# Kernel optimization log

Measured on AMD Instinct MI355X. Metric: run time of the kernel, lower is better.

Reference implementation:

```python
import jax, jax.numpy as jnp
import numpy as np

B, S, H, L = 4096, 64, 768, 5
TEMP = 0.07
BN_EPS = 1e-5


def setup_inputs() -> dict:
    key = jax.random.key(0)
    ks = jax.random.split(key, 8)
    seq = jax.random.normal(ks[0], (B, S, H), dtype=jnp.float32)
    labels = jax.random.randint(ks[1], (B,), 0, L)
    s = 1.0 / np.sqrt(H)
    return {
        'sequence_output': seq,
        'cls_gamma': jnp.ones((H,), jnp.float32),
        'cls_beta': jnp.zeros((H,), jnp.float32),
        'cls_W': jax.random.normal(ks[2], (H, H), jnp.float32) * s,
        'cls_b': jax.random.normal(ks[3], (H,), jnp.float32) * 0.01,
        'label_gamma': jnp.ones((H,), jnp.float32),
        'label_beta': jnp.zeros((H,), jnp.float32),
        'label_W': jax.random.normal(ks[4], (H, H), jnp.float32) * s,
        'label_b': jax.random.normal(ks[5], (H,), jnp.float32) * 0.01,
        'labels': labels,
    }


def _batchnorm(x, gamma, beta):
    # training-mode BatchNorm1d: biased batch stats
    m = x.mean(0)
    v = jnp.mean((x - m) ** 2, axis=0)
    return (x - m) * jax.lax.rsqrt(v + BN_EPS) * gamma + beta


def _l2norm(x):
    return x / jnp.sqrt(jnp.sum(x * x, axis=-1, keepdims=True)).clip(1e-12)


def reference(sequence_output, cls_gamma, cls_beta, cls_W, cls_b,
              label_gamma, label_beta, label_W, label_b, labels):
    z = sequence_output[:, 0, :]  # [B,H]; dropout is identity in eval
    # label token spans: 'No relation' -> positions 1:3 (mean), rest single tokens 3..6
    theta = jnp.stack([
        sequence_output[:, 1:3, :].mean(axis=1),
        sequence_output[:, 3, :],
        sequence_output[:, 4, :],
        sequence_output[:, 5, :],
        sequence_output[:, 6, :],
    ], axis=1)  # [B,L,H]
    z_cl, theta_cl = z, theta

    zp = _batchnorm(z, cls_gamma, cls_beta) @ cls_W.T + cls_b  # [B,H]
    tp = _batchnorm(theta.reshape(-1, H), label_gamma, label_beta) @ label_W.T + label_b
    tp = tp.reshape(-1, L, H)  # [B,L,H]
    logits = jnp.einsum('blh,bh->bl', tp, zp)  # [B,L]

    # ---- dual supervised contrastive loss (vectorized over the python loops) ----
    z_norm = _l2norm(z_cl)        # [B,H]
    theta_norm = _l2norm(theta_cl)  # [B,L,H]
    same = labels[:, None] == labels[None, :]          # [B,B]
    eye = jnp.eye(labels.shape[0], dtype=bool)
    pos_mask = (same & ~eye).astype(jnp.float32)       # positives (same label, j != i)
    neg_mask = (~same).astype(jnp.float32)             # negatives (different label)
    has_pos = (same & ~eye).any(axis=1)

    # l_z: anchor z_i vs theta_j[labels_i] (pos) and all theta_j[:] for diff-label j (neg)
    expS = jnp.exp(jnp.einsum('ih,jlh->ijl', z_norm, theta_norm) / TEMP)  # [B,B,L]
    expS_at_lab = jnp.take_along_axis(
        expS, jnp.broadcast_to(labels[:, None, None], expS.shape[:2] + (1,)), axis=2
    )[..., 0]  # expS[i,j,labels[i]] -> [B,B]
    pos_z = jnp.sum(expS_at_lab * pos_mask, axis=1)
    neg_z = jnp.sum(expS.sum(axis=-1) * neg_mask, axis=1)
    l_z = jnp.where(has_pos, -jnp.log(pos_z / (pos_z + neg_z + 1e-8)), 0.0).sum()

    # l_theta: anchor theta_i[labels_i] vs z_j
    anchor_theta = jnp.take_along_axis(theta_norm, labels[:, None, None], axis=1)[:, 0, :]  # [B,H]
    expT = jnp.exp(anchor_theta @ z_norm.T / TEMP)  # [B,B]
    pos_t = jnp.sum(expT * pos_mask, axis=1)
    neg_t = jnp.sum(expT * neg_mask, axis=1)
    l_t = jnp.where(has_pos, -jnp.log(pos_t / (pos_t + neg_t + 1e-8)), 0.0).sum()

    dual_loss = (l_z + l_t) / labels.shape[0]
    return logits, dual_loss
```

## Files before the change

kernel.cpp:

```cpp
#include <hip/hip_runtime.h>
#include <hip/hip_bf16.h>
#include <cstdint>
#include <cstddef>

#define B_N 4096
#define S_N 64
#define H_N 768
#define L_N 5
#define TEMP_INV (1.0f / 0.07f)
#define BN_EPS 1e-5f

typedef __attribute__((ext_vector_type(8))) short short8;
typedef __attribute__((ext_vector_type(4))) float f32x4;

__device__ __forceinline__ void async_copy16(void* lds, const void* g) {
  __builtin_amdgcn_global_load_lds(
      (const __attribute__((address_space(1))) unsigned int*)g,
      (__attribute__((address_space(3))) unsigned int*)lds, 16, 0, 0);
}

__device__ __forceinline__ unsigned short bf16b(float x) {
  __hip_bfloat16 h = __float2bfloat16(x);
  return *reinterpret_cast<unsigned short*>(&h);
}
__device__ __forceinline__ void store_bf16x4(void* p, float4 v) {
  ushort4 o = make_ushort4(bf16b(v.x), bf16b(v.y), bf16b(v.z), bf16b(v.w));
  *reinterpret_cast<ushort4*>(p) = o;
}

__device__ inline float block_reduce_sum256(float v, float* sbuf) {
#pragma unroll
  for (int off = 32; off > 0; off >>= 1) v += __shfl_down(v, off, 64);
  int lane = threadIdx.x & 63;
  int wid = threadIdx.x >> 6;
  __syncthreads();
  if (lane == 0) sbuf[wid] = v;
  __syncthreads();
  float r = 0.f;
  if (threadIdx.x == 0) r = sbuf[0] + sbuf[1] + sbuf[2] + sbuf[3];
  return r;
}

__global__ __launch_bounds__(256) void extract_kernel(
    const float* __restrict__ seq, __hip_bfloat16* __restrict__ zb,
    __hip_bfloat16* __restrict__ tb, float* __restrict__ zn_inv,
    float* __restrict__ thn_inv, float* __restrict__ sum_z,
    float* __restrict__ ssq_z, float* __restrict__ sum_t,
    float* __restrict__ ssq_t) {
  __shared__ float pr[8][6][3];
  int t = threadIdx.x;
  int wv = t >> 6, ln = t & 63;
  bool act = t < 192;
  int c4 = t * 4;
  int b0 = blockIdx.x * 8;
  float zs[4] = {}, zq[4] = {}, ts4[4] = {}, tq4[4] = {};
  for (int r = 0; r < 8; ++r) {
    int b = b0 + r;
    const float* base = seq + (size_t)b * (S_N * H_N);
    float pv[6] = {0.f, 0.f, 0.f, 0.f, 0.f, 0.f};
    if (act) {
      float4 z4 = *(const float4*)(base + c4);
      store_bf16x4(zb + (size_t)b * H_N + c4, z4);
      pv[0] = z4.x * z4.x + z4.y * z4.y + z4.z * z4.z + z4.w * z4.w;
      zs[0] += z4.x; zs[1] += z4.y; zs[2] += z4.z; zs[3] += z4.w;
      zq[0] += z4.x * z4.x; zq[1] += z4.y * z4.y;
      zq[2] += z4.z * z4.z; zq[3] += z4.w * z4.w;
#pragma unroll
      for (int l = 0; l < L_N; ++l) {
        float4 v4;
        if (l == 0) {
          float4 a4 = *(const float4*)(base + H_N + c4);
          float4 b4 = *(const float4*)(base + 2 * H_N + c4);
          v4 = make_float4(0.5f * (a4.x + b4.x), 0.5f * (a4.y + b4.y),
                           0.5f * (a4.z + b4.z), 0.5f * (a4.w + b4.w));
        } else {
          v4 = *(const float4*)(base + (size_t)(l + 2) * H_N + c4);
        }
        store_bf16x4(tb + ((size_t)b * L_N + l) * H_N + c4, v4);
        pv[1 + l] = v4.x * v4.x + v4.y * v4.y + v4.z * v4.z + v4.w * v4.w;
        ts4[0] += v4.x; ts4[1] += v4.y; ts4[2] += v4.z; ts4[3] += v4.w;
        tq4[0] += v4.x * v4.x; tq4[1] += v4.y * v4.y;
        tq4[2] += v4.z * v4.z; tq4[3] += v4.w * v4.w;
      }
    }
#pragma unroll
    for (int v = 0; v < 6; ++v) {
      float x = pv[v];
#pragma unroll
      for (int off = 32; off > 0; off >>= 1) x += __shfl_down(x, off, 64);
      if (ln == 0 && wv < 3) pr[r][v][wv] = x;
    }
  }
  __syncthreads();
  if (t < 48) {
    int r = t / 6, v = t - r * 6;
    float s = pr[r][v][0] + pr[r][v][1] + pr[r][v][2];
    float inv = 1.f / fmaxf(sqrtf(s), 1e-12f);
    int b = b0 + r;
    if (v == 0) zn_inv[b] = inv;
    else thn_inv[b * L_N + (v - 1)] = inv;
  }
  if (act) {
#pragma unroll
    for (int j = 0; j < 4; ++j) {
      atomicAdd(&sum_z[c4 + j], zs[j]);
      atomicAdd(&ssq_z[c4 + j], zq[j]);
      atomicAdd(&sum_t[c4 + j], ts4[j]);
      atomicAdd(&ssq_t[c4 + j], tq4[j]);
    }
  }
}

__global__ void count_kernel(const int* __restrict__ labels, int* __restrict__ cnt) {
  int i = blockIdx.x * 256 + threadIdx.x;
  if (i < B_N) atomicAdd(&cnt[labels[i]], 1);
}

__global__ void finalize_kernel(
    const float* __restrict__ sum_z, const float* __restrict__ ssq_z,
    const float* __restrict__ sum_t, const float* __restrict__ ssq_t,
    const float* __restrict__ g_z, const float* __restrict__ b_z,
    const float* __restrict__ g_t, const float* __restrict__ b_t,
    float* __restrict__ sz_s, float* __restrict__ sz_t,
    float* __restrict__ st_s, float* __restrict__ st_t) {
  int h = blockIdx.x * 256 + threadIdx.x;
  if (h >= H_N) return;
  {
    float m = sum_z[h] * (1.f / B_N);
    float v = ssq_z[h] * (1.f / B_N) - m * m;
    float s = g_z[h] * rsqrtf(v + BN_EPS);
    sz_s[h] = s;
    sz_t[h] = b_z[h] - m * s;
  }
  {
    float m = sum_t[h] * (1.f / (B_N * L_N));
    float v = ssq_t[h] * (1.f / (B_N * L_N)) - m * m;
    float s = g_t[h] * rsqrtf(v + BN_EPS);
    st_s[h] = s;
    st_t[h] = b_t[h] - m * s;
  }
}

__global__ __launch_bounds__(256) void prep_cls_kernel(
    const float* __restrict__ W, const float* __restrict__ szs,
    const float* __restrict__ szt, const float* __restrict__ bias,
    __hip_bfloat16* __restrict__ Wb, float* __restrict__ cprime) {
  __shared__ float sbuf[4];
  int n = blockIdx.x;
  int t = threadIdx.x;
  float dot = 0.f;
  if (t < 192) {
    int c4 = t * 4;
    const float* row = W + (size_t)n * H_N;
    float4 w4 = *(const float4*)(row + c4);
    float4 s4 = *(const float4*)(szs + c4);
    float4 t4 = *(const float4*)(szt + c4);
    store_bf16x4(Wb + (size_t)n * H_N + c4,
                 make_float4(w4.x * s4.x, w4.y * s4.y, w4.z * s4.z, w4.w * s4.w));
    dot = w4.x * t4.x + w4.y * t4.y + w4.z * t4.z + w4.w * t4.w;
  }
  float s = block_reduce_sum256(dot, sbuf);
  if (t == 0) cprime[n] = s + bias[n];
}

__global__ __launch_bounds__(256) void transpose_wl_kernel(
    const float* __restrict__ Wl, __hip_bfloat16* __restrict__ WlT) {
  __shared__ float tile[32][33];
  int t = threadIdx.x;
  int tx = t & 31, ty0 = t >> 5;
  int n0 = blockIdx.x * 32, k0 = blockIdx.y * 32;
#pragma unroll
  for (int p = 0; p < 4; ++p)
    tile[ty0 + p * 8][tx] = Wl[(size_t)(n0 + ty0 + p * 8) * H_N + k0 + tx];
  __syncthreads();
#pragma unroll
  for (int p = 0; p < 4; ++p) {
    unsigned short us = bf16b(tile[tx][ty0 + p * 8]);
    *((unsigned short*)WlT + (size_t)(k0 + ty0 + p * 8) * H_N + n0 + tx) = us;
  }
}

template <bool WRITE_BF16, bool HAS_BIAS>
__global__ __launch_bounds__(256) void gemm128_kernel(
    const __hip_bfloat16* __restrict__ A, const __hip_bfloat16* __restrict__ Bm,
    const float* __restrict__ bias, float* __restrict__ outF,
    __hip_bfloat16* __restrict__ outB) {
  __shared__ __align__(16) __hip_bfloat16 Asm[128 * 32];
  __shared__ __align__(16) __hip_bfloat16 Bsm[128 * 32];
  int tid = threadIdx.x, lane = tid & 63, wid = tid >> 6;
  int wr = wid >> 1, wc = wid & 1;
  int i0 = blockIdx.x * 128, n0 = blockIdx.y * 128;
  int llo = lane & 15, lhi = lane >> 4;
  f32x4 acc[4][4] = {};
  for (int k0 = 0; k0 < H_N; k0 += 32) {
#pragma unroll
    for (int r = 0; r < 2; ++r) {
      int s = r * 256 + wid * 64 + lane;
      int row = s >> 2, kc = (s & 3) * 8;
      size_t go = (size_t)row * H_N + k0 + kc;
      async_copy16((char*)Asm + (size_t)(r * 256 + wid * 64) * 16,
                   A + (size_t)i0 * H_N + go);
      async_copy16((char*)Bsm + (size_t)(r * 256 + wid * 64) * 16,
                   Bm + (size_t)n0 * H_N + go);
    }
    __syncthreads();
    short8 a[4], b[4];
#pragma unroll
    for (int m = 0; m < 4; ++m)
      a[m] = *(const short8*)((const char*)Asm +
                              ((wr * 64 + m * 16 + llo) * 32 + lhi * 8) * 2);
#pragma unroll
    for (int n = 0; n < 4; ++n)
      b[n] = *(const short8*)((const char*)Bsm +
                              ((wc * 64 + n * 16 + llo) * 32 + lhi * 8) * 2);
#pragma unroll
    for (int m = 0; m < 4; ++m)
#pragma unroll
      for (int n = 0; n < 4; ++n)
        acc[m][n] =
            __builtin_amdgcn_mfma_f32_16x16x32_bf16(a[m], b[n], acc[m][n], 0, 0, 0);
    __syncthreads();
  }
#pragma unroll
  for (int n = 0; n < 4; ++n) {
    int col = n0 + wc * 64 + n * 16 + llo;
    float bv = HAS_BIAS ? bias[col] : 0.f;
#pragma unroll
    for (int m = 0; m < 4; ++m) {
#pragma unroll
      for (int r = 0; r < 4; ++r) {
        int row = i0 + wr * 64 + m * 16 + lhi * 4 + r;
        float val = acc[m][n][r] + bv;
        outF[(size_t)row * H_N + col] = val;
        if (WRITE_BF16)
          outB[(size_t)row * H_N + col] = __float2bfloat16(val);
      }
    }
  }
}

__global__ __launch_bounds__(256) void logits_kernel(
    const float* __restrict__ seq, const float* __restrict__ u,
    const float* __restrict__ zp, const float* __restrict__ st_s,
    const float* __restrict__ st_t, const float* __restrict__ label_b,
    float* __restrict__ out) {
  __shared__ float sbuf[4];
  int b = blockIdx.x;
  int t = threadIdx.x;
  bool act = t < 192;
  int c4 = t * 4;
  float4 w4 = make_float4(0.f, 0.f, 0.f, 0.f);
  float apart = 0.f;
  if (act) {
    float4 u4 = *(const float4*)(u + (size_t)b * H_N + c4);
    float4 zp4 = *(const float4*)(zp + (size_t)b * H_N + c4);
    float4 ss4 = *(const float4*)(st_s + c4);
    float4 tt4 = *(const float4*)(st_t + c4);
    float4 lb4 = *(const float4*)(label_b + c4);
    w4 = make_float4(u4.x * ss4.x, u4.y * ss4.y, u4.z * ss4.z, u4.w * ss4.w);
    apart = u4.x * tt4.x + u4.y * tt4.y + u4.z * tt4.z + u4.w * tt4.w +
            zp4.x * lb4.x + zp4.y * lb4.y + zp4.z * lb4.z + zp4.w * lb4.w;
  }
  float alpha = block_reduce_sum256(apart, sbuf);
  const float* base = seq + (size_t)b * (S_N * H_N);
#pragma unroll
  for (int l = 0; l < L_N; ++l) {
    float part = 0.f;
    if (act) {
      float4 v4;
      if (l == 0) {
        float4 a4 = *(const float4*)(base + H_N + c4);
        float4 b4 = *(const float4*)(base + 2 * H_N + c4);
        v4 = make_float4(0.5f * (a4.x + b4.x), 0.5f * (a4.y + b4.y),
                         0.5f * (a4.z + b4.z), 0.5f * (a4.w + b4.w));
      } else {
        v4 = *(const float4*)(base + (size_t)(l + 2) * H_N + c4);
      }
      part = v4.x * w4.x + v4.y * w4.y + v4.z * w4.z + v4.w * w4.w;
    }
    float s = block_reduce_sum256(part, sbuf);
    if (t == 0) out[b * L_N + l] = s + alpha;
  }
}

#define NT_K 24
__global__ __launch_bounds__(256, 3) void sgemm_fused_kernel(
    const __hip_bfloat16* __restrict__ zb, const __hip_bfloat16* __restrict__ tb,
    const float* __restrict__ zn_inv, const float* __restrict__ thn_inv,
    const int* __restrict__ labels, float* __restrict__ pos_z,
    float* __restrict__ neg_z, float* __restrict__ pos_t,
    float* __restrict__ neg_t) {
  __shared__ __align__(128) char ldsbuf[2][16384];

  const int tid = threadIdx.x;
  const int lane = tid & 63, wid = tid >> 6;
  const int llo = lane & 15, lhi = lane >> 4;
  const int wr = wid >> 1, wc = wid & 1;
  const int xcd = blockIdx.x & 7;
  const int s0 = blockIdx.x >> 3;
  const int i0 = (xcd * 4 + (s0 & 3)) * 128;
  const int n0 = (s0 >> 2) * 128;

  f32x4 acc[4][4] = {};

  auto stage = [&](int c, int kt) {
#pragma unroll
    for (int h = 0; h < 2; ++h) {
      int s = h * 256 + tid;
      int R = s >> 3, sp = s & 7;
      int l = sp ^ (R & 7);
      int grow = 2 * R + (l >> 2);
      int gk = kt * 32 + (l & 3) * 8;
      int wub = (h * 256 + wid * 64) * 16;
      async_copy16(&ldsbuf[c][0] + wub, zb + (size_t)(i0 + grow) * H_N + gk);
      async_copy16(&ldsbuf[c][8192] + wub, tb + (size_t)(n0 + grow) * H_N + gk);
    }
  };

  auto fragOff = [&](int r) {
    int R = r >> 1;
    int slot = (r & 1) * 4 + lhi;
    return R * 128 + ((slot ^ (R & 7)) * 16);
  };

  stage(0, 0);
  asm volatile("s_waitcnt vmcnt(0)" ::: "memory");
  __builtin_amdgcn_s_barrier();

  for (int t = 0; t < NT_K; ++t) {
    if (t + 1 < NT_K) stage((t + 1) & 1, t + 1);
    const char* A = &ldsbuf[t & 1][0];
    const char* B = &ldsbuf[t & 1][8192];
    short8 a[4], b[4];
#pragma unroll
    for (int m = 0; m < 4; ++m) a[m] = *(const short8*)(A + fragOff(wr * 64 + m * 16 + llo));
#pragma unroll
    for (int n = 0; n < 4; ++n) b[n] = *(const short8*)(B + fragOff(wc * 64 + n * 16 + llo));
    asm volatile("s_waitcnt lgkmcnt(0)" ::: "memory");
    __builtin_amdgcn_sched_barrier(0);
    __builtin_amdgcn_s_setprio(1);
#pragma unroll
    for (int m = 0; m < 4; ++m)
#pragma unroll
      for (int n = 0; n < 4; ++n)
        acc[m][n] =
            __builtin_amdgcn_mfma_f32_16x16x32_bf16(a[m], b[n], acc[m][n], 0, 0, 0);
    __builtin_amdgcn_s_setprio(0);
    asm volatile("s_waitcnt vmcnt(0)" ::: "memory");
    __builtin_amdgcn_s_barrier();
  }
  __syncthreads();

  float* rpos = (float*)&ldsbuf[0][0];
  float* rneg = rpos + 128;
  float* cpos = rneg + 128;
  float* cneg = cpos + 128;
  float* rnorm = cneg + 128;
  float* cnorm = rnorm + 128;
  int* rowlab = (int*)(cnorm + 128);
  int* colj = rowlab + 128;
  int* coll = colj + 128;
  int* collab = coll + 128;

  if (tid < 128) {
    rowlab[tid] = labels[i0 + tid];
    rnorm[tid] = zn_inv[i0 + tid] * TEMP_INV;
    int c = n0 + tid;
    int j = c / 5;
    colj[tid] = j;
    coll[tid] = c - j * 5;
    collab[tid] = labels[j];
    cnorm[tid] = thn_inv[c];
    rpos[tid] = 0.f; rneg[tid] = 0.f; cpos[tid] = 0.f; cneg[tid] = 0.f;
  }
  __syncthreads();

  int cl[4], jg[4], lv[4], lj[4];
  float cs[4];
#pragma unroll
  for (int ni = 0; ni < 4; ++ni) {
    cl[ni] = wc * 64 + ni * 16 + llo;
    jg[ni] = colj[cl[ni]];
    lv[ni] = coll[cl[ni]];
    lj[ni] = collab[cl[ni]];
    cs[ni] = cnorm[cl[ni]];
  }
  float cpAcc[4] = {}, cnAcc[4] = {};
#pragma unroll
  for (int mi = 0; mi < 4; ++mi) {
#pragma unroll
    for (int r = 0; r < 4; ++r) {
      int rl = wr * 64 + mi * 16 + lhi * 4 + r;
      int ig = i0 + rl;
      int li = rowlab[rl];
      float rscale = rnorm[rl];
      float rp = 0.f, rn = 0.f;
#pragma unroll
      for (int ni = 0; ni < 4; ++ni) {
        float e = __expf(acc[mi][ni][r] * rscale * cs[ni]);
        bool same = (li == lj[ni]);
        bool diag = (ig == jg[ni]);
        if (same) {
          if (!diag && lv[ni] == li) { rp += e; cpAcc[ni] += e; }
        } else {
          rn += e;
          if (lv[ni] == lj[ni]) cnAcc[ni] += e;
        }
      }
      if (rp != 0.f) atomicAdd(&rpos[rl], rp);
      if (rn != 0.f) atomicAdd(&rneg[rl], rn);
    }
  }
#pragma unroll
  for (int ni = 0; ni < 4; ++ni) {
    if (cpAcc[ni] != 0.f) atomicAdd(&cpos[cl[ni]], cpAcc[ni]);
    if (cnAcc[ni] != 0.f) atomicAdd(&cneg[cl[ni]], cnAcc[ni]);
  }
  __syncthreads();
  if (tid < 128) {
    float v;
    v = rpos[tid]; if (v != 0.f) atomicAdd(&pos_z[i0 + tid], v);
    v = rneg[tid]; if (v != 0.f) atomicAdd(&neg_z[i0 + tid], v);
    int j = colj[tid];
    v = cpos[tid]; if (v != 0.f) atomicAdd(&pos_t[j], v);
    v = cneg[tid]; if (v != 0.f) atomicAdd(&neg_t[j], v);
  }
}

__global__ __launch_bounds__(256) void loss_kernel(
    const float* __restrict__ pos_z, const float* __restrict__ neg_z,
    const float* __restrict__ pos_t, const float* __restrict__ neg_t,
    const int* __restrict__ labels, const int* __restrict__ cnt,
    float* __restrict__ out_loss) {
  __shared__ float sbuf[4];
  int i = blockIdx.x * 256 + threadIdx.x;
  float term = 0.f;
  int li = labels[i];
  if (cnt[li] > 1) {
    float pz = pos_z[i], nz = neg_z[i];
    float pt = pos_t[i], nt = neg_t[i];
    term = -logf(pz / (pz + nz + 1e-8f)) - logf(pt / (pt + nt + 1e-8f));
  }
  float s = block_reduce_sum256(term, sbuf);
  if (threadIdx.x == 0) atomicAdd(out_loss, s * (1.0f / B_N));
}

extern "C" void kernel_launch(void* const* d_in, const int* in_sizes, int n_in,
                              void* d_out, int out_size, void* d_ws, size_t ws_size,
                              hipStream_t stream) {
  const float* seq = (const float*)d_in[0];
  const float* cls_gamma = (const float*)d_in[1];
  const float* cls_beta = (const float*)d_in[2];
  const float* cls_W = (const float*)d_in[3];
  const float* cls_b = (const float*)d_in[4];
  const float* label_gamma = (const float*)d_in[5];
  const float* label_beta = (const float*)d_in[6];
  const float* label_W = (const float*)d_in[7];
  const float* label_b = (const float*)d_in[8];
  const int* labels = (const int*)d_in[9];
  float* out = (float*)d_out;
  float* ws = (float*)d_ws;

  constexpr size_t OFF_SUMZ = 0;
  constexpr size_t OFF_SSQZ = 768;
  constexpr size_t OFF_SUMT = 1536;
  constexpr size_t OFF_SSQT = 2304;
  constexpr size_t OFF_POSZ = 3072;
  constexpr size_t OFF_NEGZ = 7168;
  constexpr size_t OFF_POST = 11264;
  constexpr size_t OFF_NEGT = 15360;
  constexpr size_t OFF_CNT = 19456;
  constexpr size_t ZERO_FLOATS = 19464;
  constexpr size_t OFF_SZS = 19464;
  constexpr size_t OFF_SZT = 20232;
  constexpr size_t OFF_STS = 21000;
  constexpr size_t OFF_STT = 21768;
  constexpr size_t OFF_ZNI = 22536;
  constexpr size_t OFF_TNI = 26632;
  constexpr size_t OFF_CPRIME = 47112;
  constexpr size_t OFF_ZP = 47880;
  constexpr size_t OFF_U = OFF_ZP + (size_t)B_N * H_N;
  constexpr size_t F32_END = OFF_U + (size_t)B_N * H_N;
  constexpr size_t BYTE_ZB = F32_END * sizeof(float);
  constexpr size_t BYTE_TB = BYTE_ZB + (size_t)B_N * H_N * 2;
  constexpr size_t BYTE_ZPB = BYTE_TB + (size_t)B_N * L_N * H_N * 2;
  constexpr size_t BYTE_WCB = BYTE_ZPB + (size_t)B_N * H_N * 2;
  constexpr size_t BYTE_WLT = BYTE_WCB + (size_t)H_N * H_N * 2;
  constexpr size_t TOTAL_BYTES = BYTE_WLT + (size_t)H_N * H_N * 2;
  if (ws_size < TOTAL_BYTES) return;

  __hip_bfloat16* zb = (__hip_bfloat16*)((char*)d_ws + BYTE_ZB);
  __hip_bfloat16* tb = (__hip_bfloat16*)((char*)d_ws + BYTE_TB);
  __hip_bfloat16* zpb = (__hip_bfloat16*)((char*)d_ws + BYTE_ZPB);
  __hip_bfloat16* wcb = (__hip_bfloat16*)((char*)d_ws + BYTE_WCB);
  __hip_bfloat16* wlt = (__hip_bfloat16*)((char*)d_ws + BYTE_WLT);

  hipMemsetAsync(d_ws, 0, ZERO_FLOATS * sizeof(float), stream);
  hipMemsetAsync((char*)d_out + (size_t)B_N * L_N * sizeof(float), 0, sizeof(float),
                 stream);

  extract_kernel<<<512, 256, 0, stream>>>(seq, zb, tb, ws + OFF_ZNI, ws + OFF_TNI,
                                          ws + OFF_SUMZ, ws + OFF_SSQZ,
                                          ws + OFF_SUMT, ws + OFF_SSQT);
  count_kernel<<<16, 256, 0, stream>>>(labels, (int*)(ws + OFF_CNT));
  finalize_kernel<<<3, 256, 0, stream>>>(
      ws + OFF_SUMZ, ws + OFF_SSQZ, ws + OFF_SUMT, ws + OFF_SSQT, cls_gamma,
      cls_beta, label_gamma, label_beta, ws + OFF_SZS, ws + OFF_SZT, ws + OFF_STS,
      ws + OFF_STT);
  prep_cls_kernel<<<H_N, 256, 0, stream>>>(cls_W, ws + OFF_SZS, ws + OFF_SZT, cls_b,
                                           wcb, ws + OFF_CPRIME);
  transpose_wl_kernel<<<dim3(24, 24), 256, 0, stream>>>(label_W, wlt);
  gemm128_kernel<true, true><<<dim3(32, 6), 256, 0, stream>>>(
      zb, wcb, ws + OFF_CPRIME, ws + OFF_ZP, zpb);
  gemm128_kernel<false, false><<<dim3(32, 6), 256, 0, stream>>>(
      zpb, wlt, nullptr, ws + OFF_U, nullptr);
  logits_kernel<<<B_N, 256, 0, stream>>>(seq, ws + OFF_U, ws + OFF_ZP, ws + OFF_STS,
                                         ws + OFF_STT, label_b, out);
  sgemm_fused_kernel<<<5120, 256, 0, stream>>>(
      zb, tb, ws + OFF_ZNI, ws + OFF_TNI, labels, ws + OFF_POSZ, ws + OFF_NEGZ,
      ws + OFF_POST, ws + OFF_NEGT);
  loss_kernel<<<16, 256, 0, stream>>>(ws + OFF_POSZ, ws + OFF_NEGZ, ws + OFF_POST,
                                      ws + OFF_NEGT, labels,
                                      (const int*)(ws + OFF_CNT),
                                      out + (size_t)B_N * L_N);
}
```

Baseline: 461.1 us.

## Shrink sgemm column tile, fuse label count into extract, read bf16 theta in logits

```diff
diff --git a/kernel.cpp b/kernel.cpp
--- a/kernel.cpp
+++ b/kernel.cpp
@@ -27,6 +27,10 @@
   ushort4 o = make_ushort4(bf16b(v.x), bf16b(v.y), bf16b(v.z), bf16b(v.w));
   *reinterpret_cast<ushort4*>(p) = o;
 }
+__device__ __forceinline__ float bf2f(unsigned short u) {
+  unsigned int x = ((unsigned int)u) << 16;
+  return *reinterpret_cast<float*>(&x);
+}
 
 __device__ inline float block_reduce_sum256(float v, float* sbuf) {
 #pragma unroll
@@ -46,13 +50,15 @@
     __hip_bfloat16* __restrict__ tb, float* __restrict__ zn_inv,
     float* __restrict__ thn_inv, float* __restrict__ sum_z,
     float* __restrict__ ssq_z, float* __restrict__ sum_t,
-    float* __restrict__ ssq_t) {
+    float* __restrict__ ssq_t, const int* __restrict__ labels,
+    int* __restrict__ cnt) {
   __shared__ float pr[8][6][3];
   int t = threadIdx.x;
   int wv = t >> 6, ln = t & 63;
   bool act = t < 192;
   int c4 = t * 4;
   int b0 = blockIdx.x * 8;
+  if (t < 8) atomicAdd(&cnt[labels[b0 + t]], 1);
   float zs[4] = {}, zq[4] = {}, ts4[4] = {}, tq4[4] = {};
   for (int r = 0; r < 8; ++r) {
     int b = b0 + r;
@@ -109,11 +115,6 @@
       atomicAdd(&ssq_t[c4 + j], tq4[j]);
     }
   }
-}
-
-__global__ void count_kernel(const int* __restrict__ labels, int* __restrict__ cnt) {
-  int i = blockIdx.x * 256 + threadIdx.x;
-  if (i < B_N) atomicAdd(&cnt[labels[i]], 1);
 }
 
 __global__ void finalize_kernel(
@@ -240,7 +241,7 @@
 }
 
 __global__ __launch_bounds__(256) void logits_kernel(
-    const float* __restrict__ seq, const float* __restrict__ u,
+    const __hip_bfloat16* __restrict__ tb, const float* __restrict__ u,
     const float* __restrict__ zp, const float* __restrict__ st_s,
     const float* __restrict__ st_t, const float* __restrict__ label_b,
     float* __restrict__ out) {
@@ -262,21 +263,14 @@
             zp4.x * lb4.x + zp4.y * lb4.y + zp4.z * lb4.z + zp4.w * lb4.w;
   }
   float alpha = block_reduce_sum256(apart, sbuf);
-  const float* base = seq + (size_t)b * (S_N * H_N);
 #pragma unroll
   for (int l = 0; l < L_N; ++l) {
     float part = 0.f;
     if (act) {
-      float4 v4;
-      if (l == 0) {
-        float4 a4 = *(const float4*)(base + H_N + c4);
-        float4 b4 = *(const float4*)(base + 2 * H_N + c4);
-        v4 = make_float4(0.5f * (a4.x + b4.x), 0.5f * (a4.y + b4.y),
-                         0.5f * (a4.z + b4.z), 0.5f * (a4.w + b4.w));
-      } else {
-        v4 = *(const float4*)(base + (size_t)(l + 2) * H_N + c4);
-      }
-      part = v4.x * w4.x + v4.y * w4.y + v4.z * w4.z + v4.w * w4.w;
+      ushort4 tv = *(const ushort4*)((const unsigned short*)tb +
+                                     ((size_t)b * L_N + l) * H_N + c4);
+      part = bf2f(tv.x) * w4.x + bf2f(tv.y) * w4.y + bf2f(tv.z) * w4.z +
+             bf2f(tv.w) * w4.w;
     }
     float s = block_reduce_sum256(part, sbuf);
     if (t == 0) out[b * L_N + l] = s + alpha;
@@ -284,13 +278,13 @@
 }
 
 #define NT_K 24
-__global__ __launch_bounds__(256, 3) void sgemm_fused_kernel(
+__global__ __launch_bounds__(256, 4) void sgemm_fused_kernel(
     const __hip_bfloat16* __restrict__ zb, const __hip_bfloat16* __restrict__ tb,
     const float* __restrict__ zn_inv, const float* __restrict__ thn_inv,
     const int* __restrict__ labels, float* __restrict__ pos_z,
     float* __restrict__ neg_z, float* __restrict__ pos_t,
     float* __restrict__ neg_t) {
-  __shared__ __align__(128) char ldsbuf[2][16384];
+  __shared__ __align__(128) char ldsbuf[2][12288];
 
   const int tid = threadIdx.x;
   const int lane = tid & 63, wid = tid >> 6;
@@ -299,9 +293,9 @@
   const int xcd = blockIdx.x & 7;
   const int s0 = blockIdx.x >> 3;
   const int i0 = (xcd * 4 + (s0 & 3)) * 128;
-  const int n0 = (s0 >> 2) * 128;
-
-  f32x4 acc[4][4] = {};
+  const int n0 = (s0 >> 2) * 64;
+
+  f32x4 acc[4][2] = {};
 
   auto stage = [&](int c, int kt) {
 #pragma unroll
@@ -313,6 +307,14 @@
       int gk = kt * 32 + (l & 3) * 8;
       int wub = (h * 256 + wid * 64) * 16;
       async_copy16(&ldsbuf[c][0] + wub, zb + (size_t)(i0 + grow) * H_N + gk);
+    }
+    {
+      int s = tid;
+      int R = s >> 3, sp = s & 7;
+      int l = sp ^ (R & 7);
+      int grow = 2 * R + (l >> 2);
+      int gk = kt * 32 + (l & 3) * 8;
+      int wub = (wid * 64) * 16;
       async_copy16(&ldsbuf[c][8192] + wub, tb + (size_t)(n0 + grow) * H_N + gk);
     }
   };
@@ -331,18 +333,20 @@
     if (t + 1 < NT_K) stage((t + 1) & 1, t + 1);
     const char* A = &ldsbuf[t & 1][0];
     const char* B = &ldsbuf[t & 1][8192];
-    short8 a[4], b[4];
-#pragma unroll
-    for (int m = 0; m < 4; ++m) a[m] = *(const short8*)(A + fragOff(wr * 64 + m * 16 + llo));
-#pragma unroll
-    for (int n = 0; n < 4; ++n) b[n] = *(const short8*)(B + fragOff(wc * 64 + n * 16 + llo));
+    short8 a[4], b[2];
+#pragma unroll
+    for (int m = 0; m < 4; ++m)
+      a[m] = *(const short8*)(A + fragOff(wr * 64 + m * 16 + llo));
+#pragma unroll
+    for (int n = 0; n < 2; ++n)
+      b[n] = *(const short8*)(B + fragOff(wc * 32 + n * 16 + llo));
     asm volatile("s_waitcnt lgkmcnt(0)" ::: "memory");
     __builtin_amdgcn_sched_barrier(0);
     __builtin_amdgcn_s_setprio(1);
 #pragma unroll
     for (int m = 0; m < 4; ++m)
 #pragma unroll
-      for (int n = 0; n < 4; ++n)
+      for (int n = 0; n < 2; ++n)
         acc[m][n] =
             __builtin_amdgcn_mfma_f32_16x16x32_bf16(a[m], b[n], acc[m][n], 0, 0, 0);
     __builtin_amdgcn_s_setprio(0);
@@ -353,39 +357,42 @@
 
   float* rpos = (float*)&ldsbuf[0][0];
   float* rneg = rpos + 128;
-  float* cpos = rneg + 128;
-  float* cneg = cpos + 128;
-  float* rnorm = cneg + 128;
-  float* cnorm = rnorm + 128;
-  int* rowlab = (int*)(cnorm + 128);
+  float* rnorm = rneg + 128;
+  float* cpos = rnorm + 128;
+  float* cneg = cpos + 64;
+  float* cnorm = cneg + 64;
+  int* rowlab = (int*)(cnorm + 64);
   int* colj = rowlab + 128;
-  int* coll = colj + 128;
-  int* collab = coll + 128;
+  int* coll = colj + 64;
+  int* collab = coll + 64;
 
   if (tid < 128) {
     rowlab[tid] = labels[i0 + tid];
     rnorm[tid] = zn_inv[i0 + tid] * TEMP_INV;
+    rpos[tid] = 0.f; rneg[tid] = 0.f;
+  }
+  if (tid < 64) {
     int c = n0 + tid;
     int j = c / 5;
     colj[tid] = j;
     coll[tid] = c - j * 5;
     collab[tid] = labels[j];
     cnorm[tid] = thn_inv[c];
-    rpos[tid] = 0.f; rneg[tid] = 0.f; cpos[tid] = 0.f; cneg[tid] = 0.f;
-  }
-  __syncthreads();
-
-  int cl[4], jg[4], lv[4], lj[4];
-  float cs[4];
-#pragma unroll
-  for (int ni = 0; ni < 4; ++ni) {
-    cl[ni] = wc * 64 + ni * 16 + llo;
+    cpos[tid] = 0.f; cneg[tid] = 0.f;
+  }
+  __syncthreads();
+
+  int cl[2], jg[2], lv[2], lj[2];
+  float cs[2];
+#pragma unroll
+  for (int ni = 0; ni < 2; ++ni) {
+    cl[ni] = wc * 32 + ni * 16 + llo;
     jg[ni] = colj[cl[ni]];
     lv[ni] = coll[cl[ni]];
     lj[ni] = collab[cl[ni]];
     cs[ni] = cnorm[cl[ni]];
   }
-  float cpAcc[4] = {}, cnAcc[4] = {};
+  float cpAcc[2] = {}, cnAcc[2] = {};
 #pragma unroll
   for (int mi = 0; mi < 4; ++mi) {
 #pragma unroll
@@ -396,7 +403,7 @@
       float rscale = rnorm[rl];
       float rp = 0.f, rn = 0.f;
 #pragma unroll
-      for (int ni = 0; ni < 4; ++ni) {
+      for (int ni = 0; ni < 2; ++ni) {
         float e = __expf(acc[mi][ni][r] * rscale * cs[ni]);
         bool same = (li == lj[ni]);
         bool diag = (ig == jg[ni]);
@@ -412,7 +419,7 @@
     }
   }
 #pragma unroll
-  for (int ni = 0; ni < 4; ++ni) {
+  for (int ni = 0; ni < 2; ++ni) {
     if (cpAcc[ni] != 0.f) atomicAdd(&cpos[cl[ni]], cpAcc[ni]);
     if (cnAcc[ni] != 0.f) atomicAdd(&cneg[cl[ni]], cnAcc[ni]);
   }
@@ -421,7 +428,10 @@
     float v;
     v = rpos[tid]; if (v != 0.f) atomicAdd(&pos_z[i0 + tid], v);
     v = rneg[tid]; if (v != 0.f) atomicAdd(&neg_z[i0 + tid], v);
+  }
+  if (tid < 64) {
     int j = colj[tid];
+    float v;
     v = cpos[tid]; if (v != 0.f) atomicAdd(&pos_t[j], v);
     v = cneg[tid]; if (v != 0.f) atomicAdd(&neg_t[j], v);
   }
@@ -501,8 +511,8 @@
 
   extract_kernel<<<512, 256, 0, stream>>>(seq, zb, tb, ws + OFF_ZNI, ws + OFF_TNI,
                                           ws + OFF_SUMZ, ws + OFF_SSQZ,
-                                          ws + OFF_SUMT, ws + OFF_SSQT);
-  count_kernel<<<16, 256, 0, stream>>>(labels, (int*)(ws + OFF_CNT));
+                                          ws + OFF_SUMT, ws + OFF_SSQT, labels,
+                                          (int*)(ws + OFF_CNT));
   finalize_kernel<<<3, 256, 0, stream>>>(
       ws + OFF_SUMZ, ws + OFF_SSQZ, ws + OFF_SUMT, ws + OFF_SSQT, cls_gamma,
       cls_beta, label_gamma, label_beta, ws + OFF_SZS, ws + OFF_SZT, ws + OFF_STS,
@@ -514,9 +524,9 @@
       zb, wcb, ws + OFF_CPRIME, ws + OFF_ZP, zpb);
   gemm128_kernel<false, false><<<dim3(32, 6), 256, 0, stream>>>(
       zpb, wlt, nullptr, ws + OFF_U, nullptr);
-  logits_kernel<<<B_N, 256, 0, stream>>>(seq, ws + OFF_U, ws + OFF_ZP, ws + OFF_STS,
+  logits_kernel<<<B_N, 256, 0, stream>>>(tb, ws + OFF_U, ws + OFF_ZP, ws + OFF_STS,
                                          ws + OFF_STT, label_b, out);
-  sgemm_fused_kernel<<<5120, 256, 0, stream>>>(
+  sgemm_fused_kernel<<<10240, 256, 0, stream>>>(
       zb, tb, ws + OFF_ZNI, ws + OFF_TNI, labels, ws + OFF_POSZ, ws + OFF_NEGZ,
       ws + OFF_POST, ws + OFF_NEGT);
   loss_kernel<<<16, 256, 0, stream>>>(ws + OFF_POSZ, ws + OFF_NEGZ, ws + OFF_POST,
```

New measurement: 601.6 us. 30.5% more time.

## Trim idle threads, fuse label count into extract, read bf16 theta in logits

Applied to the files above, without the earlier changes.

```diff
diff --git a/kernel.cpp b/kernel.cpp
--- a/kernel.cpp
+++ b/kernel.cpp
@@ -27,6 +27,10 @@
   ushort4 o = make_ushort4(bf16b(v.x), bf16b(v.y), bf16b(v.z), bf16b(v.w));
   *reinterpret_cast<ushort4*>(p) = o;
 }
+__device__ __forceinline__ float bf2f(unsigned short u) {
+  unsigned int x = ((unsigned int)u) << 16;
+  return *reinterpret_cast<float*>(&x);
+}
 
 __device__ inline float block_reduce_sum256(float v, float* sbuf) {
 #pragma unroll
@@ -41,24 +45,38 @@
   return r;
 }
 
-__global__ __launch_bounds__(256) void extract_kernel(
+__device__ inline float block_reduce_sum192(float v, float* sbuf) {
+#pragma unroll
+  for (int off = 32; off > 0; off >>= 1) v += __shfl_down(v, off, 64);
+  int lane = threadIdx.x & 63;
+  int wid = threadIdx.x >> 6;
+  __syncthreads();
+  if (lane == 0) sbuf[wid] = v;
+  __syncthreads();
+  float r = 0.f;
+  if (threadIdx.x == 0) r = sbuf[0] + sbuf[1] + sbuf[2];
+  return r;
+}
+
+__global__ __launch_bounds__(192) void extract_kernel(
     const float* __restrict__ seq, __hip_bfloat16* __restrict__ zb,
     __hip_bfloat16* __restrict__ tb, float* __restrict__ zn_inv,
     float* __restrict__ thn_inv, float* __restrict__ sum_z,
     float* __restrict__ ssq_z, float* __restrict__ sum_t,
-    float* __restrict__ ssq_t) {
-  __shared__ float pr[8][6][3];
+    float* __restrict__ ssq_t, const int* __restrict__ labels,
+    int* __restrict__ cnt) {
+  __shared__ float pr[4][6][3];
   int t = threadIdx.x;
   int wv = t >> 6, ln = t & 63;
-  bool act = t < 192;
   int c4 = t * 4;
-  int b0 = blockIdx.x * 8;
+  int b0 = blockIdx.x * 4;
+  if (t < 4) atomicAdd(&cnt[labels[b0 + t]], 1);
   float zs[4] = {}, zq[4] = {}, ts4[4] = {}, tq4[4] = {};
-  for (int r = 0; r < 8; ++r) {
+  for (int r = 0; r < 4; ++r) {
     int b = b0 + r;
     const float* base = seq + (size_t)b * (S_N * H_N);
-    float pv[6] = {0.f, 0.f, 0.f, 0.f, 0.f, 0.f};
-    if (act) {
+    float pv[6];
+    {
       float4 z4 = *(const float4*)(base + c4);
       store_bf16x4(zb + (size_t)b * H_N + c4, z4);
       pv[0] = z4.x * z4.x + z4.y * z4.y + z4.z * z4.z + z4.w * z4.w;
@@ -88,11 +106,11 @@
       float x = pv[v];
 #pragma unroll
       for (int off = 32; off > 0; off >>= 1) x += __shfl_down(x, off, 64);
-      if (ln == 0 && wv < 3) pr[r][v][wv] = x;
+      if (ln == 0) pr[r][v][wv] = x;
     }
   }
   __syncthreads();
-  if (t < 48) {
+  if (t < 24) {
     int r = t / 6, v = t - r * 6;
     float s = pr[r][v][0] + pr[r][v][1] + pr[r][v][2];
     float inv = 1.f / fmaxf(sqrtf(s), 1e-12f);
@@ -100,20 +118,13 @@
     if (v == 0) zn_inv[b] = inv;
     else thn_inv[b * L_N + (v - 1)] = inv;
   }
-  if (act) {
-#pragma unroll
-    for (int j = 0; j < 4; ++j) {
-      atomicAdd(&sum_z[c4 + j], zs[j]);
-      atomicAdd(&ssq_z[c4 + j], zq[j]);
-      atomicAdd(&sum_t[c4 + j], ts4[j]);
-      atomicAdd(&ssq_t[c4 + j], tq4[j]);
-    }
-  }
-}
-
-__global__ void count_kernel(const int* __restrict__ labels, int* __restrict__ cnt) {
-  int i = blockIdx.x * 256 + threadIdx.x;
-  if (i < B_N) atomicAdd(&cnt[labels[i]], 1);
+#pragma unroll
+  for (int j = 0; j < 4; ++j) {
+    atomicAdd(&sum_z[c4 + j], zs[j]);
+    atomicAdd(&ssq_z[c4 + j], zq[j]);
+    atomicAdd(&sum_t[c4 + j], ts4[j]);
+    atomicAdd(&ssq_t[c4 + j], tq4[j]);
+  }
 }
 
 __global__ void finalize_kernel(
@@ -141,25 +152,22 @@
   }
 }
 
-__global__ __launch_bounds__(256) void prep_cls_kernel(
+__global__ __launch_bounds__(192) void prep_cls_kernel(
     const float* __restrict__ W, const float* __restrict__ szs,
     const float* __restrict__ szt, const float* __restrict__ bias,
     __hip_bfloat16* __restrict__ Wb, float* __restrict__ cprime) {
-  __shared__ float sbuf[4];
+  __shared__ float sbuf[3];
   int n = blockIdx.x;
   int t = threadIdx.x;
-  float dot = 0.f;
-  if (t < 192) {
-    int c4 = t * 4;
-    const float* row = W + (size_t)n * H_N;
-    float4 w4 = *(const float4*)(row + c4);
-    float4 s4 = *(const float4*)(szs + c4);
-    float4 t4 = *(const float4*)(szt + c4);
-    store_bf16x4(Wb + (size_t)n * H_N + c4,
-                 make_float4(w4.x * s4.x, w4.y * s4.y, w4.z * s4.z, w4.w * s4.w));
-    dot = w4.x * t4.x + w4.y * t4.y + w4.z * t4.z + w4.w * t4.w;
-  }
-  float s = block_reduce_sum256(dot, sbuf);
+  int c4 = t * 4;
+  const float* row = W + (size_t)n * H_N;
+  float4 w4 = *(const float4*)(row + c4);
+  float4 s4 = *(const float4*)(szs + c4);
+  float4 t4 = *(const float4*)(szt + c4);
+  store_bf16x4(Wb + (size_t)n * H_N + c4,
+               make_float4(w4.x * s4.x, w4.y * s4.y, w4.z * s4.z, w4.w * s4.w));
+  float dot = w4.x * t4.x + w4.y * t4.y + w4.z * t4.z + w4.w * t4.w;
+  float s = block_reduce_sum192(dot, sbuf);
   if (t == 0) cprime[n] = s + bias[n];
 }
 
@@ -239,46 +247,31 @@
   }
 }
 
-__global__ __launch_bounds__(256) void logits_kernel(
-    const float* __restrict__ seq, const float* __restrict__ u,
+__global__ __launch_bounds__(192) void logits_kernel(
+    const __hip_bfloat16* __restrict__ tb, const float* __restrict__ u,
     const float* __restrict__ zp, const float* __restrict__ st_s,
     const float* __restrict__ st_t, const float* __restrict__ label_b,
     float* __restrict__ out) {
-  __shared__ float sbuf[4];
+  __shared__ float sbuf[3];
   int b = blockIdx.x;
   int t = threadIdx.x;
-  bool act = t < 192;
   int c4 = t * 4;
-  float4 w4 = make_float4(0.f, 0.f, 0.f, 0.f);
-  float apart = 0.f;
-  if (act) {
-    float4 u4 = *(const float4*)(u + (size_t)b * H_N + c4);
-    float4 zp4 = *(const float4*)(zp + (size_t)b * H_N + c4);
-    float4 ss4 = *(const float4*)(st_s + c4);
-    float4 tt4 = *(const float4*)(st_t + c4);
-    float4 lb4 = *(const float4*)(label_b + c4);
-    w4 = make_float4(u4.x * ss4.x, u4.y * ss4.y, u4.z * ss4.z, u4.w * ss4.w);
-    apart = u4.x * tt4.x + u4.y * tt4.y + u4.z * tt4.z + u4.w * tt4.w +
-            zp4.x * lb4.x + zp4.y * lb4.y + zp4.z * lb4.z + zp4.w * lb4.w;
-  }
-  float alpha = block_reduce_sum256(apart, sbuf);
-  const float* base = seq + (size_t)b * (S_N * H_N);
+  float4 u4 = *(const float4*)(u + (size_t)b * H_N + c4);
+  float4 zp4 = *(const float4*)(zp + (size_t)b * H_N + c4);
+  float4 ss4 = *(const float4*)(st_s + c4);
+  float4 tt4 = *(const float4*)(st_t + c4);
+  float4 lb4 = *(const float4*)(label_b + c4);
+  float4 w4 = make_float4(u4.x * ss4.x, u4.y * ss4.y, u4.z * ss4.z, u4.w * ss4.w);
+  float apart = u4.x * tt4.x + u4.y * tt4.y + u4.z * tt4.z + u4.w * tt4.w +
+                zp4.x * lb4.x + zp4.y * lb4.y + zp4.z * lb4.z + zp4.w * lb4.w;
+  float alpha = block_reduce_sum192(apart, sbuf);
 #pragma unroll
   for (int l = 0; l < L_N; ++l) {
-    float part = 0.f;
-    if (act) {
-      float4 v4;
-      if (l == 0) {
-        float4 a4 = *(const float4*)(base + H_N + c4);
-        float4 b4 = *(const float4*)(base + 2 * H_N + c4);
-        v4 = make_float4(0.5f * (a4.x + b4.x), 0.5f * (a4.y + b4.y),
-                         0.5f * (a4.z + b4.z), 0.5f * (a4.w + b4.w));
-      } else {
-        v4 = *(const float4*)(base + (size_t)(l + 2) * H_N + c4);
-      }
-      part = v4.x * w4.x + v4.y * w4.y + v4.z * w4.z + v4.w * w4.w;
-    }
-    float s = block_reduce_sum256(part, sbuf);
+    ushort4 tv = *(const ushort4*)((const unsigned short*)tb +
+                                   ((size_t)b * L_N + l) * H_N + c4);
+    float part = bf2f(tv.x) * w4.x + bf2f(tv.y) * w4.y + bf2f(tv.z) * w4.z +
+                 bf2f(tv.w) * w4.w;
+    float s = block_reduce_sum192(part, sbuf);
     if (t == 0) out[b * L_N + l] = s + alpha;
   }
 }
@@ -499,22 +492,22 @@
   hipMemsetAsync((char*)d_out + (size_t)B_N * L_N * sizeof(float), 0, sizeof(float),
                  stream);
 
-  extract_kernel<<<512, 256, 0, stream>>>(seq, zb, tb, ws + OFF_ZNI, ws + OFF_TNI,
-                                          ws + OFF_SUMZ, ws + OFF_SSQZ,
-                                          ws + OFF_SUMT, ws + OFF_SSQT);
-  count_kernel<<<16, 256, 0, stream>>>(labels, (int*)(ws + OFF_CNT));
+  extract_kernel<<<1024, 192, 0, stream>>>(seq, zb, tb, ws + OFF_ZNI, ws + OFF_TNI,
+                                           ws + OFF_SUMZ, ws + OFF_SSQZ,
+                                           ws + OFF_SUMT, ws + OFF_SSQT, labels,
+                                           (int*)(ws + OFF_CNT));
   finalize_kernel<<<3, 256, 0, stream>>>(
       ws + OFF_SUMZ, ws + OFF_SSQZ, ws + OFF_SUMT, ws + OFF_SSQT, cls_gamma,
       cls_beta, label_gamma, label_beta, ws + OFF_SZS, ws + OFF_SZT, ws + OFF_STS,
       ws + OFF_STT);
-  prep_cls_kernel<<<H_N, 256, 0, stream>>>(cls_W, ws + OFF_SZS, ws + OFF_SZT, cls_b,
+  prep_cls_kernel<<<H_N, 192, 0, stream>>>(cls_W, ws + OFF_SZS, ws + OFF_SZT, cls_b,
                                            wcb, ws + OFF_CPRIME);
   transpose_wl_kernel<<<dim3(24, 24), 256, 0, stream>>>(label_W, wlt);
   gemm128_kernel<true, true><<<dim3(32, 6), 256, 0, stream>>>(
       zb, wcb, ws + OFF_CPRIME, ws + OFF_ZP, zpb);
   gemm128_kernel<false, false><<<dim3(32, 6), 256, 0, stream>>>(
       zpb, wlt, nullptr, ws + OFF_U, nullptr);
-  logits_kernel<<<B_N, 256, 0, stream>>>(seq, ws + OFF_U, ws + OFF_ZP, ws + OFF_STS,
+  logits_kernel<<<B_N, 192, 0, stream>>>(tb, ws + OFF_U, ws + OFF_ZP, ws + OFF_STS,
                                          ws + OFF_STT, label_b, out);
   sgemm_fused_kernel<<<5120, 256, 0, stream>>>(
       zb, tb, ws + OFF_ZNI, ws + OFF_TNI, labels, ws + OFF_POSZ, ws + OFF_NEGZ,
```

Measured after the change: 499.1 us. 1.08x slower.
